# Optimization experiments

Hardware: AMD Instinct MI355X
Metric: run time of the kernel (lower is better)

Reference implementation:

```python
import jax, jax.numpy as jnp
import numpy as np

B, L, F = 4096, 50, 128      # batch, hist_l, per-step feature dim (in_dim // hist_l)
H, E = 8, 128                # h_att, emb_dim
DQK = E                      # per-head q/k dim = (emb_dim*h_att)//h_att
DV = E // H                  # per-head v dim = emb_dim // h_att


def setup_inputs() -> dict:
    key = jax.random.key(0)
    ks = jax.random.split(key, 7)
    s_f = 1.0 / np.sqrt(F)
    return {
        "hid": jax.random.normal(ks[0], (B, L * F), dtype=jnp.float32),
        "Wq": jax.random.normal(ks[1], (H, F, DQK), dtype=jnp.float32) * s_f,
        "bq": jax.random.normal(ks[2], (H, DQK), dtype=jnp.float32) * 0.01,
        "Wk": jax.random.normal(ks[3], (H, F, DQK), dtype=jnp.float32) * s_f,
        "bk": jax.random.normal(ks[4], (H, DQK), dtype=jnp.float32) * 0.01,
        "Wv": jax.random.normal(ks[5], (H, F, DV), dtype=jnp.float32) * s_f,
        "bv": jax.random.normal(ks[6], (H, DV), dtype=jnp.float32) * 0.01,
    }


def reference(hid, Wq, bq, Wk, bk, Wv, bv):
    b = hid.shape[0]
    x = hid.reshape(b, L, F)                                   # [B, L, F]
    # all heads batched: q,k [B, H, L, DQK], v [B, H, L, DV]
    q = jnp.einsum("blf,hfe->bhle", x, Wq) + bq[None, :, None, :]
    k = jnp.einsum("blf,hfe->bhle", x, Wk) + bk[None, :, None, :]
    v = jnp.einsum("blf,hfv->bhlv", x, Wv) + bv[None, :, None, :]
    scores = jnp.einsum("bhle,bhme->bhlm", q, k)               # [B, H, L, L]
    scores = jnp.where(scores > 0, scores, 0.1 * scores)       # leaky_relu(0.1)
    # original uses nn.Softmax(dim=1) on [B, L, L] -> normalize over ROW axis (axis 2 here)
    att = jax.nn.softmax(scores, axis=2)
    out = jnp.einsum("bhlm,bhmv->bhlv", att, v)                # [B, H, L, DV]
    out = jnp.transpose(out, (0, 2, 1, 3)).reshape(b, L, H * DV)  # concat heads last-dim
    return jax.nn.relu(out).reshape(b, -1)                     # [B, L*emb_dim]
```

## Files before the change

### kernel.cpp

```cpp
#include <hip/hip_runtime.h>
#include <math.h>

#define NB   4096
#define LL   50
#define FF   128
#define HH   8
#define DVn  16

typedef __attribute__((ext_vector_type(8))) short bf16x8;
typedef __attribute__((ext_vector_type(4))) float f32x4;

__device__ __forceinline__ ushort bf_hi(float x) {
    uint u = __float_as_uint(x);
    uint r = u + 0x7FFFu + ((u >> 16) & 1u);
    return (ushort)(r >> 16);
}
__device__ __forceinline__ float bf_f(ushort b) { return __uint_as_float(((uint)b) << 16); }

__global__ __launch_bounds__(256)
void pack_w(const float* __restrict__ Wq, const float* __restrict__ bq,
            const float* __restrict__ Wk, const float* __restrict__ bk,
            const float* __restrict__ Wv, ushort* __restrict__ wp)
{
    __shared__ float sw[128*129 + 16*129];
    const int t    = threadIdx.x;
    const int lane = t & 63;
    const int ks   = t >> 6;
    const int h    = blockIdx.x / 10;
    const int tile = blockIdx.x % 10;
    const int c    = lane & 15;
    const int f0   = ks*32 + (lane >> 4)*8;

    float val[8];
    #pragma unroll
    for (int j = 0; j < 8; ++j) val[j] = 0.f;

    if (tile < 8) {
        const float* wq = Wq + (size_t)h*FF*FF;
        const float* wk = Wk + (size_t)h*FF*FF;
        float* wqs = sw;
        float* wks = sw + 128*129;
        for (int i = t; i < 128*128; i += 256)
            wqs[(i>>7)*129 + (i&127)] = wq[i];
        for (int i = t; i < 16*128;  i += 256)
            wks[(i>>7)*129 + (i&127)] = wk[(size_t)(tile*16 + (i>>7))*FF + (i&127)];
        __syncthreads();
        for (int e = 0; e < FF; ++e) {
            float kv = wks[c*129 + e];
            #pragma unroll
            for (int j = 0; j < 8; ++j) val[j] += wqs[(f0+j)*129 + e] * kv;
        }
    } else if (tile == 8) {
        const float* wq = Wq + (size_t)h*FF*FF;
        const float* wk = Wk + (size_t)h*FF*FF;
        float pu[8], pv[8];
        #pragma unroll
        for (int j = 0; j < 8; ++j) { pu[j] = 0.f; pv[j] = 0.f; }
        for (int ee = 0; ee < 8; ++ee) {
            int e = c*8 + ee;
            float bkk = bk[h*FF + e], bqq = bq[h*FF + e];
            #pragma unroll
            for (int j = 0; j < 8; ++j) {
                pu[j] += wq[(size_t)(f0+j)*FF + e] * bkk;
                pv[j] += wk[(size_t)(f0+j)*FF + e] * bqq;
            }
        }
        #pragma unroll
        for (int m = 1; m < 16; m <<= 1) {
            #pragma unroll
            for (int j = 0; j < 8; ++j) {
                pu[j] += __shfl_xor(pu[j], m);
                pv[j] += __shfl_xor(pv[j], m);
            }
        }
        if (c == 0) {
            #pragma unroll
            for (int j = 0; j < 8; ++j) val[j] = pu[j];
        } else if (c == 1) {
            #pragma unroll
            for (int j = 0; j < 8; ++j) val[j] = pv[j];
        }
        if (ks == 0) {
            float s = bq[h*FF + lane*2]*bk[h*FF + lane*2]
                    + bq[h*FF + lane*2 + 1]*bk[h*FF + lane*2 + 1];
            #pragma unroll
            for (int m = 1; m < 64; m <<= 1) s += __shfl_xor(s, m);
            if (lane == 0) ((float*)(wp + 327680))[h] = s;
        }
    } else {
        const float* wv = Wv + (size_t)h*FF*DVn;
        #pragma unroll
        for (int j = 0; j < 8; ++j) val[j] = wv[(size_t)(f0+j)*DVn + c];
    }

    ushort hi[8], lo[8];
    #pragma unroll
    for (int j = 0; j < 8; ++j) {
        ushort hb = bf_hi(val[j]);
        hi[j] = hb;
        lo[j] = bf_hi(val[j] - bf_f(hb));
    }
    size_t base = (size_t)h*40960 + (size_t)tile*4096 + ks*1024 + lane*8;
    *(ushort4*)(wp + base)       = make_ushort4(hi[0],hi[1],hi[2],hi[3]);
    *(ushort4*)(wp + base + 4)   = make_ushort4(hi[4],hi[5],hi[6],hi[7]);
    *(ushort4*)(wp + base + 512) = make_ushort4(lo[0],lo[1],lo[2],lo[3]);
    *(ushort4*)(wp + base + 516) = make_ushort4(lo[4],lo[5],lo[6],lo[7]);
}

#define PX    528
#define XL0   0
#define XH0   8448
#define TH0   8448
#define TDEL  8448
#define SATT0 8448
#define VF0   25344
#define SATTP 88
#define TU0   13184
#define TV0   13248
#define LDS_FLOATS 13312

__global__ __launch_bounds__(256, 3)
void attn_fused(const float* __restrict__ hid, const ushort* __restrict__ wp,
                const float* __restrict__ ccp, const float* __restrict__ bv,
                float* __restrict__ out)
{
    __shared__ __align__(16) float lds[LDS_FLOATS];
    ushort* us = (ushort*)lds;
    float*  tu = lds + TU0;
    float*  tv = lds + TV0;

    const int t    = threadIdx.x;
    const int b    = blockIdx.x;
    const int lane = t & 63;
    const int w    = t >> 6;
    const int c16  = lane & 15;
    const int quad = lane >> 4;
    const int lsw8 = (lane ^ (((lane >> 4) & 1) << 1)) * 8;

    {
        const float4* src = (const float4*)(hid + (size_t)b * (LL*FF));
        for (int i = t; i < 1600; i += 256) {
            float4 v = src[i];
            int l = i >> 5, f0 = (i & 31) * 4;
            int slot = ((l>>4)*4 + (f0>>5))*PX + ((l&15) + 16*((f0&31)>>3))*8 + (f0&7);
            ushort4 hv, lv;
            hv.x = bf_hi(v.x); lv.x = bf_hi(v.x - bf_f(hv.x));
            hv.y = bf_hi(v.y); lv.y = bf_hi(v.y - bf_f(hv.y));
            hv.z = bf_hi(v.z); lv.z = bf_hi(v.z - bf_f(hv.z));
            hv.w = bf_hi(v.w); lv.w = bf_hi(v.w - bf_f(hv.w));
            *(ushort4*)(us + XH0 + slot) = hv;
            *(ushort4*)(us + XL0 + slot) = lv;
        }
    }
    __syncthreads();

    bf16x8 xh[16];
    #pragma unroll
    for (int i = 0; i < 16; ++i)
        xh[i] = *(const bf16x8*)(us + XH0 + i*PX + lane*8);
    __syncthreads();

    #pragma unroll 1
    for (int h = 0; h < HH; ++h) {
        f32x4 aT[4][2], aU, aV;
        #pragma unroll
        for (int m = 0; m < 4; ++m) {
            aT[m][0] = (f32x4){0.f,0.f,0.f,0.f};
            aT[m][1] = (f32x4){0.f,0.f,0.f,0.f};
        }
        aU = (f32x4){0.f,0.f,0.f,0.f};
        aV = (f32x4){0.f,0.f,0.f,0.f};

        const ushort* wb = wp + (size_t)h*40960 + lane*8;
        #define WFRG(tt,kk,pp) (*(const bf16x8*)(wb + (size_t)(tt)*4096 + (kk)*1024 + (pp)*512))

        #pragma unroll
        for (int ks = 0; ks < 4; ++ks) {
            bf16x8 m0h = WFRG(2*w,   ks, 0), m0l = WFRG(2*w,   ks, 1);
            bf16x8 m1h = WFRG(2*w+1, ks, 0), m1l = WFRG(2*w+1, ks, 1);
            bf16x8 uvh = WFRG(8, ks, 0);
            bf16x8 vvh = WFRG(9, ks, 0);
            #pragma unroll
            for (int mt = 0; mt < 4; ++mt) {
                bf16x8 ah = xh[mt*4 + ks];
                bf16x8 al = *(const bf16x8*)(us + XL0 + (mt*4 + ks)*PX + lane*8);
                aT[mt][0] = __builtin_amdgcn_mfma_f32_16x16x32_bf16(ah, m0h, aT[mt][0], 0,0,0);
                aT[mt][0] = __builtin_amdgcn_mfma_f32_16x16x32_bf16(ah, m0l, aT[mt][0], 0,0,0);
                aT[mt][0] = __builtin_amdgcn_mfma_f32_16x16x32_bf16(al, m0h, aT[mt][0], 0,0,0);
                aT[mt][1] = __builtin_amdgcn_mfma_f32_16x16x32_bf16(ah, m1h, aT[mt][1], 0,0,0);
                aT[mt][1] = __builtin_amdgcn_mfma_f32_16x16x32_bf16(ah, m1l, aT[mt][1], 0,0,0);
                aT[mt][1] = __builtin_amdgcn_mfma_f32_16x16x32_bf16(al, m1h, aT[mt][1], 0,0,0);
                if (mt == w) {
                    aU = __builtin_amdgcn_mfma_f32_16x16x32_bf16(ah, uvh, aU, 0,0,0);
                    aV = __builtin_amdgcn_mfma_f32_16x16x32_bf16(ah, vvh, aV, 0,0,0);
                    aV = __builtin_amdgcn_mfma_f32_16x16x32_bf16(al, vvh, aV, 0,0,0);
                }
            }
        }

        {
            const int jj   = c16 & 7;
            const int hi16 = c16 >> 3;
            const int sw2  = hi16 << 1;
            #pragma unroll
            for (int nt = 0; nt < 2; ++nt) {
                #pragma unroll
                for (int mt = 0; mt < 4; ++mt) {
                    int pb = (mt*4 + w)*PX + jj;
                    #pragma unroll
                    for (int r = 0; r < 4; ++r) {
                        int grp = ((quad*4 + r) ^ sw2) + 16*(nt*2 + hi16);
                        int idx = pb + grp*8;
                        float tval = aT[mt][nt][r];
                        ushort th_ = bf_hi(tval);
                        us[TH0 + idx]        = th_;
                        us[TH0 + TDEL + idx] = bf_hi(tval - bf_f(th_));
                    }
                }
            }
            if (c16 < 2) {
                float* dst = (c16 == 0) ? tu : tv;
                #pragma unroll
                for (int r = 0; r < 4; ++r) dst[w*16 + quad*4 + r] = aU[r];
            }
            float bvv = bv[h*DVn + c16];
            int ksp = w >> 1;
            #pragma unroll
            for (int r = 0; r < 4; ++r) {
                int m  = w*16 + quad*4 + r;
                int mm = (w&1)*16 + quad*4 + r;
                int Lp = c16 + 16*(mm >> 3);
                us[VF0 + ksp*512 + Lp*8 + (mm & 7)] = (m < LL) ? bf_hi(aV[r] + bvv) : (ushort)0;
            }
        }
        __syncthreads();

        f32x4 sc[4];
        #pragma unroll
        for (int m = 0; m < 4; ++m) sc[m] = (f32x4){0.f,0.f,0.f,0.f};

        #pragma unroll
        for (int cw = 0; cw < 4; ++cw) if (w == cw) {
            #pragma unroll
            for (int ks = 0; ks < 4; ++ks) {
                bf16x8 bh = xh[cw*4 + ks];
                bf16x8 bl = *(const bf16x8*)(us + XL0 + (cw*4 + ks)*PX + lane*8);
                #pragma unroll
                for (int mt = 0; mt < 4; ++mt) {
                    const ushort* tb = us + TH0 + (mt*4 + ks)*PX + lsw8;
                    bf16x8 th = *(const bf16x8*)tb;
                    bf16x8 tl = *(const bf16x8*)(tb + TDEL);
                    sc[mt] = __builtin_amdgcn_mfma_f32_16x16x32_bf16(th, bh, sc[mt], 0,0,0);
                    sc[mt] = __builtin_amdgcn_mfma_f32_16x16x32_bf16(tl, bh, sc[mt], 0,0,0);
                    sc[mt] = __builtin_amdgcn_mfma_f32_16x16x32_bf16(th, bl, sc[mt], 0,0,0);
                }
            }
        }

        const float cc  = ccp[h];
        const int mcol  = w*16 + c16;
        const float tvv = tv[mcol] + cc;
        float mx = -INFINITY;
        #pragma unroll
        for (int mt = 0; mt < 4; ++mt)
            #pragma unroll
            for (int r = 0; r < 4; ++r) {
                int l = mt*16 + quad*4 + r;
                float s = sc[mt][r] + tu[l] + tvv;
                s = (s > 0.f) ? s : 0.1f*s;
                sc[mt][r] = s;
                if (l < LL) mx = fmaxf(mx, s);
            }
        mx = fmaxf(mx, __shfl_xor(mx, 16));
        mx = fmaxf(mx, __shfl_xor(mx, 32));
        float sum = 0.f;
        #pragma unroll
        for (int mt = 0; mt < 4; ++mt)
            #pragma unroll
            for (int r = 0; r < 4; ++r) {
                int l = mt*16 + quad*4 + r;
                float p = (l < LL) ? __expf(sc[mt][r] - mx) : 0.f;
                sc[mt][r] = p;
                sum += p;
            }
        sum += __shfl_xor(sum, 16);
        sum += __shfl_xor(sum, 32);
        float inv = 1.0f / sum;

        __syncthreads();

        #pragma unroll
        for (int mt = 0; mt < 4; ++mt)
            #pragma unroll
            for (int r = 0; r < 4; ++r) {
                int l = mt*16 + quad*4 + r;
                us[SATT0 + l*SATTP + mcol] = (mcol < LL) ? bf_hi(sc[mt][r] * inv) : (ushort)0;
            }
        __syncthreads();

        f32x4 ao = (f32x4){0.f,0.f,0.f,0.f};
        #pragma unroll
        for (int ksp = 0; ksp < 2; ++ksp) {
            bf16x8 af = *(const bf16x8*)(us + SATT0 + (w*16 + c16)*SATTP + ksp*32 + quad*8);
            bf16x8 bf = *(const bf16x8*)(us + VF0 + ksp*512 + lane*8);
            ao = __builtin_amdgcn_mfma_f32_16x16x32_bf16(af, bf, ao, 0,0,0);
        }
        #pragma unroll
        for (int r = 0; r < 4; ++r) {
            int l = w*16 + quad*4 + r;
            if (l < LL)
                out[(size_t)b*(LL*FF) + l*FF + h*DVn + c16] = fmaxf(ao[r], 0.f);
        }
        __syncthreads();
    }
}

extern "C" void kernel_launch(void* const* d_in, const int* in_sizes, int n_in,
                              void* d_out, int out_size, void* d_ws, size_t ws_size,
                              hipStream_t stream)
{
    const float* hid = (const float*)d_in[0];
    const float* Wq  = (const float*)d_in[1];
    const float* bq  = (const float*)d_in[2];
    const float* Wk  = (const float*)d_in[3];
    const float* bk  = (const float*)d_in[4];
    const float* Wv  = (const float*)d_in[5];
    const float* bv  = (const float*)d_in[6];
    float* o    = (float*)d_out;
    ushort* wp  = (ushort*)d_ws;
    const float* ccp = (const float*)(wp + 327680);

    pack_w<<<dim3(80), dim3(256), 0, stream>>>(Wq, bq, Wk, bk, Wv, wp);
    attn_fused<<<dim3(NB), dim3(256), 0, stream>>>(hid, wp, ccp, bv, o);
}
```

Baseline: 505.4 us.

## Transpose bilinear Wq·Wkᵀ product layout, split pack_w across more blocks, truncate bf16 splits

```diff
diff --git a/kernel.cpp b/kernel.cpp
--- a/kernel.cpp
+++ b/kernel.cpp
@@ -17,19 +17,21 @@
 }
 __device__ __forceinline__ float bf_f(ushort b) { return __uint_as_float(((uint)b) << 16); }
 
-__global__ __launch_bounds__(256)
+__global__ __launch_bounds__(64)
 void pack_w(const float* __restrict__ Wq, const float* __restrict__ bq,
             const float* __restrict__ Wk, const float* __restrict__ bk,
             const float* __restrict__ Wv, ushort* __restrict__ wp)
 {
-    __shared__ float sw[128*129 + 16*129];
-    const int t    = threadIdx.x;
-    const int lane = t & 63;
-    const int ks   = t >> 6;
-    const int h    = blockIdx.x / 10;
-    const int tile = blockIdx.x % 10;
+    __shared__ float sw[48*129];
+    const int lane = threadIdx.x;
+    const int bx   = blockIdx.x;
+    const int h    = bx / 40;
+    const int r40  = bx % 40;
+    const int tile = r40 >> 2;
+    const int ks   = r40 & 3;
     const int c    = lane & 15;
-    const int f0   = ks*32 + (lane >> 4)*8;
+    const int quad = lane >> 4;
+    const int f0   = ks*32 + quad*8;
 
     float val[8];
     #pragma unroll
@@ -39,16 +41,17 @@
         const float* wq = Wq + (size_t)h*FF*FF;
         const float* wk = Wk + (size_t)h*FF*FF;
         float* wqs = sw;
-        float* wks = sw + 128*129;
-        for (int i = t; i < 128*128; i += 256)
-            wqs[(i>>7)*129 + (i&127)] = wq[i];
-        for (int i = t; i < 16*128;  i += 256)
-            wks[(i>>7)*129 + (i&127)] = wk[(size_t)(tile*16 + (i>>7))*FF + (i&127)];
+        float* wks = sw + 16*129;
+        for (int i = lane; i < 16*128; i += 64)
+            wqs[(i>>7)*129 + (i&127)] = wq[(size_t)(tile*16 + (i>>7))*FF + (i&127)];
+        for (int i = lane; i < 32*128; i += 64)
+            wks[(i>>7)*129 + (i&127)] = wk[(size_t)(ks*32 + (i>>7))*FF + (i&127)];
         __syncthreads();
         for (int e = 0; e < FF; ++e) {
-            float kv = wks[c*129 + e];
-            #pragma unroll
-            for (int j = 0; j < 8; ++j) val[j] += wqs[(f0+j)*129 + e] * kv;
+            float qv = wqs[c*129 + e];
+            #pragma unroll
+            for (int j = 0; j < 8; ++j)
+                val[j] += wks[(quad*8 + j)*129 + e] * qv;
         }
     } else if (tile == 8) {
         const float* wq = Wq + (size_t)h*FF*FF;
@@ -110,11 +113,11 @@
 #define PX    528
 #define XL0   0
 #define XH0   8448
-#define TH0   8448
-#define TDEL  8448
+#define GB0   8448
+#define GDEL  8448
 #define SATT0 8448
+#define SATTP 88
 #define VF0   25344
-#define SATTP 88
 #define TU0   13184
 #define TV0   13248
 #define LDS_FLOATS 13312
@@ -135,7 +138,6 @@
     const int w    = t >> 6;
     const int c16  = lane & 15;
     const int quad = lane >> 4;
-    const int lsw8 = (lane ^ (((lane >> 4) & 1) << 1)) * 8;
 
     {
         const float4* src = (const float4*)(hid + (size_t)b * (LL*FF));
@@ -144,10 +146,15 @@
             int l = i >> 5, f0 = (i & 31) * 4;
             int slot = ((l>>4)*4 + (f0>>5))*PX + ((l&15) + 16*((f0&31)>>3))*8 + (f0&7);
             ushort4 hv, lv;
-            hv.x = bf_hi(v.x); lv.x = bf_hi(v.x - bf_f(hv.x));
-            hv.y = bf_hi(v.y); lv.y = bf_hi(v.y - bf_f(hv.y));
-            hv.z = bf_hi(v.z); lv.z = bf_hi(v.z - bf_f(hv.z));
-            hv.w = bf_hi(v.w); lv.w = bf_hi(v.w - bf_f(hv.w));
+            uint ux;
+            ux = __float_as_uint(v.x); hv.x = (ushort)(ux>>16);
+            lv.x = (ushort)(__float_as_uint(v.x - __uint_as_float(ux & 0xFFFF0000u))>>16);
+            ux = __float_as_uint(v.y); hv.y = (ushort)(ux>>16);
+            lv.y = (ushort)(__float_as_uint(v.y - __uint_as_float(ux & 0xFFFF0000u))>>16);
+            ux = __float_as_uint(v.z); hv.z = (ushort)(ux>>16);
+            lv.z = (ushort)(__float_as_uint(v.z - __uint_as_float(ux & 0xFFFF0000u))>>16);
+            ux = __float_as_uint(v.w); hv.w = (ushort)(ux>>16);
+            lv.w = (ushort)(__float_as_uint(v.w - __uint_as_float(ux & 0xFFFF0000u))>>16);
             *(ushort4*)(us + XH0 + slot) = hv;
             *(ushort4*)(us + XL0 + slot) = lv;
         }
@@ -162,12 +169,11 @@
 
     #pragma unroll 1
     for (int h = 0; h < HH; ++h) {
-        f32x4 aT[4][2], aU, aV;
-        #pragma unroll
-        for (int m = 0; m < 4; ++m) {
-            aT[m][0] = (f32x4){0.f,0.f,0.f,0.f};
-            aT[m][1] = (f32x4){0.f,0.f,0.f,0.f};
-        }
+        f32x4 aG[2][4], aU, aV;
+        #pragma unroll
+        for (int i = 0; i < 2; ++i)
+            #pragma unroll
+            for (int m = 0; m < 4; ++m) aG[i][m] = (f32x4){0.f,0.f,0.f,0.f};
         aU = (f32x4){0.f,0.f,0.f,0.f};
         aV = (f32x4){0.f,0.f,0.f,0.f};
 
@@ -182,40 +188,43 @@
             bf16x8 vvh = WFRG(9, ks, 0);
             #pragma unroll
             for (int mt = 0; mt < 4; ++mt) {
-                bf16x8 ah = xh[mt*4 + ks];
-                bf16x8 al = *(const bf16x8*)(us + XL0 + (mt*4 + ks)*PX + lane*8);
-                aT[mt][0] = __builtin_amdgcn_mfma_f32_16x16x32_bf16(ah, m0h, aT[mt][0], 0,0,0);
-                aT[mt][0] = __builtin_amdgcn_mfma_f32_16x16x32_bf16(ah, m0l, aT[mt][0], 0,0,0);
-                aT[mt][0] = __builtin_amdgcn_mfma_f32_16x16x32_bf16(al, m0h, aT[mt][0], 0,0,0);
-                aT[mt][1] = __builtin_amdgcn_mfma_f32_16x16x32_bf16(ah, m1h, aT[mt][1], 0,0,0);
-                aT[mt][1] = __builtin_amdgcn_mfma_f32_16x16x32_bf16(ah, m1l, aT[mt][1], 0,0,0);
-                aT[mt][1] = __builtin_amdgcn_mfma_f32_16x16x32_bf16(al, m1h, aT[mt][1], 0,0,0);
+                bf16x8 bh = xh[mt*4 + ks];
+                bf16x8 bl = *(const bf16x8*)(us + XL0 + (mt*4 + ks)*PX + lane*8);
+                aG[0][mt] = __builtin_amdgcn_mfma_f32_16x16x32_bf16(m0h, bh, aG[0][mt], 0,0,0);
+                aG[0][mt] = __builtin_amdgcn_mfma_f32_16x16x32_bf16(m0l, bh, aG[0][mt], 0,0,0);
+                aG[0][mt] = __builtin_amdgcn_mfma_f32_16x16x32_bf16(m0h, bl, aG[0][mt], 0,0,0);
+                aG[1][mt] = __builtin_amdgcn_mfma_f32_16x16x32_bf16(m1h, bh, aG[1][mt], 0,0,0);
+                aG[1][mt] = __builtin_amdgcn_mfma_f32_16x16x32_bf16(m1l, bh, aG[1][mt], 0,0,0);
+                aG[1][mt] = __builtin_amdgcn_mfma_f32_16x16x32_bf16(m1h, bl, aG[1][mt], 0,0,0);
                 if (mt == w) {
-                    aU = __builtin_amdgcn_mfma_f32_16x16x32_bf16(ah, uvh, aU, 0,0,0);
-                    aV = __builtin_amdgcn_mfma_f32_16x16x32_bf16(ah, vvh, aV, 0,0,0);
-                    aV = __builtin_amdgcn_mfma_f32_16x16x32_bf16(al, vvh, aV, 0,0,0);
+                    aU = __builtin_amdgcn_mfma_f32_16x16x32_bf16(bh, uvh, aU, 0,0,0);
+                    aV = __builtin_amdgcn_mfma_f32_16x16x32_bf16(bh, vvh, aV, 0,0,0);
+                    aV = __builtin_amdgcn_mfma_f32_16x16x32_bf16(bl, vvh, aV, 0,0,0);
                 }
             }
         }
 
         {
-            const int jj   = c16 & 7;
-            const int hi16 = c16 >> 3;
-            const int sw2  = hi16 << 1;
-            #pragma unroll
-            for (int nt = 0; nt < 2; ++nt) {
+            #pragma unroll
+            for (int i = 0; i < 2; ++i) {
                 #pragma unroll
                 for (int mt = 0; mt < 4; ++mt) {
-                    int pb = (mt*4 + w)*PX + jj;
-                    #pragma unroll
-                    for (int r = 0; r < 4; ++r) {
-                        int grp = ((quad*4 + r) ^ sw2) + 16*(nt*2 + hi16);
-                        int idx = pb + grp*8;
-                        float tval = aT[mt][nt][r];
-                        ushort th_ = bf_hi(tval);
-                        us[TH0 + idx]        = th_;
-                        us[TH0 + TDEL + idx] = bf_hi(tval - bf_f(th_));
-                    }
+                    uint u0 = __float_as_uint(aG[i][mt][0]);
+                    uint u1 = __float_as_uint(aG[i][mt][1]);
+                    uint u2 = __float_as_uint(aG[i][mt][2]);
+                    uint u3 = __float_as_uint(aG[i][mt][3]);
+                    uint hw0 = (u0>>16) | (u1 & 0xFFFF0000u);
+                    uint hw1 = (u2>>16) | (u3 & 0xFFFF0000u);
+                    float l0 = aG[i][mt][0] - __uint_as_float(u0 & 0xFFFF0000u);
+                    float l1 = aG[i][mt][1] - __uint_as_float(u1 & 0xFFFF0000u);
+                    float l2 = aG[i][mt][2] - __uint_as_float(u2 & 0xFFFF0000u);
+                    float l3 = aG[i][mt][3] - __uint_as_float(u3 & 0xFFFF0000u);
+                    uint lw0 = (__float_as_uint(l0)>>16) | (__float_as_uint(l1) & 0xFFFF0000u);
+                    uint lw1 = (__float_as_uint(l2)>>16) | (__float_as_uint(l3) & 0xFFFF0000u);
+                    ushort* dst = us + GB0 + (mt*4 + w)*PX
+                                  + (c16 + 16*(2*i + (quad>>1)))*8 + (quad&1)*4;
+                    *(uint2*)dst          = make_uint2(hw0, hw1);
+                    *(uint2*)(dst + GDEL) = make_uint2(lw0, lw1);
                 }
             }
             if (c16 < 2) {
@@ -240,20 +249,17 @@
         for (int m = 0; m < 4; ++m) sc[m] = (f32x4){0.f,0.f,0.f,0.f};
 
         #pragma unroll
-        for (int cw = 0; cw < 4; ++cw) if (w == cw) {
-            #pragma unroll
-            for (int ks = 0; ks < 4; ++ks) {
-                bf16x8 bh = xh[cw*4 + ks];
-                bf16x8 bl = *(const bf16x8*)(us + XL0 + (cw*4 + ks)*PX + lane*8);
-                #pragma unroll
-                for (int mt = 0; mt < 4; ++mt) {
-                    const ushort* tb = us + TH0 + (mt*4 + ks)*PX + lsw8;
-                    bf16x8 th = *(const bf16x8*)tb;
-                    bf16x8 tl = *(const bf16x8*)(tb + TDEL);
-                    sc[mt] = __builtin_amdgcn_mfma_f32_16x16x32_bf16(th, bh, sc[mt], 0,0,0);
-                    sc[mt] = __builtin_amdgcn_mfma_f32_16x16x32_bf16(tl, bh, sc[mt], 0,0,0);
-                    sc[mt] = __builtin_amdgcn_mfma_f32_16x16x32_bf16(th, bl, sc[mt], 0,0,0);
-                }
+        for (int ks = 0; ks < 4; ++ks) {
+            const ushort* gb = us + GB0 + (w*4 + ks)*PX + lane*8;
+            bf16x8 gh = *(const bf16x8*)gb;
+            bf16x8 gl = *(const bf16x8*)(gb + GDEL);
+            #pragma unroll
+            for (int mt = 0; mt < 4; ++mt) {
+                bf16x8 ah = xh[mt*4 + ks];
+                bf16x8 al = *(const bf16x8*)(us + XL0 + (mt*4 + ks)*PX + lane*8);
+                sc[mt] = __builtin_amdgcn_mfma_f32_16x16x32_bf16(ah, gh, sc[mt], 0,0,0);
+                sc[mt] = __builtin_amdgcn_mfma_f32_16x16x32_bf16(al, gh, sc[mt], 0,0,0);
+                sc[mt] = __builtin_amdgcn_mfma_f32_16x16x32_bf16(ah, gl, sc[mt], 0,0,0);
             }
         }
 
@@ -262,15 +268,18 @@
         const float tvv = tv[mcol] + cc;
         float mx = -INFINITY;
         #pragma unroll
-        for (int mt = 0; mt < 4; ++mt)
+        for (int mt = 0; mt < 4; ++mt) {
+            const float4 tq = *(const float4*)(tu + mt*16 + quad*4);
+            float tqa[4] = {tq.x, tq.y, tq.z, tq.w};
             #pragma unroll
             for (int r = 0; r < 4; ++r) {
                 int l = mt*16 + quad*4 + r;
-                float s = sc[mt][r] + tu[l] + tvv;
+                float s = sc[mt][r] + tqa[r] + tvv;
                 s = (s > 0.f) ? s : 0.1f*s;
                 sc[mt][r] = s;
                 if (l < LL) mx = fmaxf(mx, s);
             }
+        }
         mx = fmaxf(mx, __shfl_xor(mx, 16));
         mx = fmaxf(mx, __shfl_xor(mx, 32));
         float sum = 0.f;
@@ -330,6 +339,6 @@
     ushort* wp  = (ushort*)d_ws;
     const float* ccp = (const float*)(wp + 327680);
 
-    pack_w<<<dim3(80), dim3(256), 0, stream>>>(Wq, bq, Wk, bk, Wv, wp);
+    pack_w<<<dim3(320), dim3(64), 0, stream>>>(Wq, bq, Wk, bk, Wv, wp);
     attn_fused<<<dim3(NB), dim3(256), 0, stream>>>(hid, wp, ccp, bv, o);
 }
```

Result: faster. 478.7 us (-5.3%).
